# Optimization experiments

Measured on AMD Instinct MI355X. Metric: run time of the kernel, lower is better.

## Reference

```python
import jax, jax.numpy as jnp
import numpy as np

B, N, H, D2 = 2, 2048, 16, 64


def setup_inputs() -> dict:
    key = jax.random.key(0)
    k1, k2, k3 = jax.random.split(key, 3)
    keys = jax.random.normal(k1, (B, N, H, D2), dtype=jnp.float32)
    queries = jax.random.normal(k2, (B, N, H, D2), dtype=jnp.float32)
    values = jax.random.normal(k3, (B, N, H, D2), dtype=jnp.float32)
    return {"keys": keys, "queries": queries, "values": values}


def reference(keys, queries, values):
    b, n, h, d2 = keys.shape
    # Faithful to the original: torch uses .reshape (NOT transpose) to go
    # (b, n, h, d2) -> (b, h, n, d2), a pure memory reinterpretation.
    q = queries.reshape(b, h, n, d2)
    k = keys.reshape(b, h, n, d2)
    v = values.reshape(b, h, n, d2)
    scale = 1.0 / (d2 ** 0.5)
    # [b, h, n, n] attention scores
    scores = jnp.einsum('bhqd,bhkd->bhqk', q, k) * scale
    # causal mask: upper triangle (diagonal=1) set to -inf
    causal = jnp.triu(jnp.ones((n, n), dtype=bool), k=1)
    scores = jnp.where(causal, -jnp.inf, scores)
    attn = jax.nn.softmax(scores, axis=-1)
    out = jnp.einsum('bhqk,bhkd->bhqd', attn, v)
    return out.reshape(b, n, h, d2)
```

## Files before the change

kernel.cpp:

```cpp
#include <hip/hip_runtime.h>


typedef short  short4v __attribute__((ext_vector_type(4)));
typedef short  short8v __attribute__((ext_vector_type(8)));
typedef float  float4v __attribute__((ext_vector_type(4)));
typedef float  float8v __attribute__((ext_vector_type(8)));

#define NQ 2048
#define DD 64
#define KT 64
#define KP 72
#define VP 72

union U2 { unsigned int u[2]; short4v s; };
union U4 { unsigned int u[4]; short8v s; };

static __device__ __forceinline__ unsigned int pktr(float lo, float hi) {
    return __builtin_amdgcn_perm(__builtin_bit_cast(unsigned int, hi),
                                 __builtin_bit_cast(unsigned int, lo),
                                 0x07060302);
}
static __device__ __forceinline__ unsigned int pkrn(float lo, float hi) {
    unsigned int a = __builtin_bit_cast(unsigned int, hi) + 0x8000u;
    unsigned int b = __builtin_bit_cast(unsigned int, lo) + 0x8000u;
    return __builtin_amdgcn_perm(a, b, 0x07060302);
}

__global__ __launch_bounds__(512, 4) void mha_fwd_kernel(
    const float* __restrict__ Kg,
    const float* __restrict__ Qg,
    const float* __restrict__ Vg,
    float* __restrict__ Og)
{
    __shared__ __align__(16) unsigned short Klds[2][KT * KP];
    __shared__ __align__(16) unsigned short Vt[2][DD * VP];

    const int t    = threadIdx.x;
    const int lane = t & 63;
    const int wave = t >> 6;
    const int col  = lane & 15;
    const int quad = lane >> 4;

    const int b  = blockIdx.x;
    const int bh = (b & 7) * 4 + ((b >> 3) & 3);
    const int h  = b >> 5;
    const int p  = (h < 8) ? h : 23 - h;

    const int T    = (wave < 4) ? (31 - p) : p;
    const int q0   = T * 64 + (wave & 3) * 16;
    const int qg   = q0 + col;
    const int kmax = T * 64;
    const int nt   = 32 - p;

    const size_t base = (size_t)bh * NQ * DD;
    const float* Qp = Qg + base;
    const float* Kp = Kg + base;
    const float* Vp = Vg + base;
    float*       Op = Og + base;

    const float sscale = 0.125f * 1.4426950408889634f;

    const int kr = t >> 3, kc = (t & 7) * 8;
    const int vd = t & 63, vg = (t >> 6) * 8;

    short8v qf0, qf1;
    {
        float8v a = *(const float8v*)(Qp + (size_t)qg * DD + quad * 8);
        float8v c = *(const float8v*)(Qp + (size_t)qg * DD + 32 + quad * 8);
        U4 w0, w1;
#pragma unroll
        for (int i = 0; i < 4; ++i) {
            w0.u[i] = pkrn(a[2 * i] * sscale, a[2 * i + 1] * sscale);
            w1.u[i] = pkrn(c[2 * i] * sscale, c[2 * i + 1] * sscale);
        }
        qf0 = w0.s;
        qf1 = w1.s;
    }

    float l_i = 0.0f;
    float4v o[4];
#pragma unroll
    for (int d = 0; d < 4; ++d) o[d] = (float4v){0.f, 0.f, 0.f, 0.f};

    {
        float8v ka = *(const float8v*)(Kp + (size_t)kr * DD + kc);
        float vr[8];
#pragma unroll
        for (int i = 0; i < 8; ++i) vr[i] = Vp[(size_t)(vg + i) * DD + vd];
        U4 wk, wv;
#pragma unroll
        for (int i = 0; i < 4; ++i) {
            wk.u[i] = pktr(ka[2 * i], ka[2 * i + 1]);
            wv.u[i] = pktr(vr[2 * i], vr[2 * i + 1]);
        }
        *(short8v*)&Klds[0][kr * KP + kc] = wk.s;
        *(short8v*)&Vt[0][vd * VP + vg]   = wv.s;
    }
    __syncthreads();

    for (int it = 0; it < nt; ++it) {
        const int cur   = it & 1;
        const int kb    = it * KT;
        const bool stage = (it + 1 < nt);

        float8v ka;
        float vr[8];
        if (stage) {
            const int nkb = kb + KT;
            ka = *(const float8v*)(Kp + (size_t)(nkb + kr) * DD + kc);
#pragma unroll
            for (int i = 0; i < 8; ++i)
                vr[i] = Vp[(size_t)(nkb + vg + i) * DD + vd];
        }

        if (kb <= kmax) {
            __builtin_amdgcn_s_setprio(1);

            float4v sT[4];
#pragma unroll
            for (int u = 0; u < 4; ++u) {
                short8v kf0 = *(const short8v*)&Klds[cur][(u * 16 + col) * KP + quad * 8];
                short8v kf1 = *(const short8v*)&Klds[cur][(u * 16 + col) * KP + 32 + quad * 8];
                sT[u] = (float4v){0.f, 0.f, 0.f, 0.f};
                sT[u] = __builtin_amdgcn_mfma_f32_16x16x32_bf16(kf0, qf0, sT[u], 0, 0, 0);
                sT[u] = __builtin_amdgcn_mfma_f32_16x16x32_bf16(kf1, qf1, sT[u], 0, 0, 0);
            }

            if (kb == kmax) {
#pragma unroll
                for (int u = 0; u < 4; ++u)
#pragma unroll
                    for (int r = 0; r < 4; ++r) {
                        const int key = kb + u * 16 + quad * 4 + r;
                        if (key > qg) sT[u][r] = -3.0e38f;
                    }
            }

            short4v pf[4];
#pragma unroll
            for (int u = 0; u < 4; ++u) {
#pragma unroll
                for (int r = 0; r < 4; ++r) {
                    sT[u][r] = exp2f(sT[u][r]);
                    l_i += sT[u][r];
                }
                U2 w;
                w.u[0] = pktr(sT[u][0], sT[u][1]);
                w.u[1] = pktr(sT[u][2], sT[u][3]);
                pf[u] = w.s;
            }

#pragma unroll
            for (int d = 0; d < 4; ++d) {
#pragma unroll
                for (int u = 0; u < 4; ++u) {
                    short4v vf = *(const short4v*)&Vt[cur][(d * 16 + col) * VP + u * 16 + quad * 4];
                    o[d] = __builtin_amdgcn_mfma_f32_16x16x16bf16_1k(pf[u], vf, o[d], 0, 0, 0);
                }
            }

            __builtin_amdgcn_s_setprio(0);
        }

        if (stage) {
            U4 wk, wv;
#pragma unroll
            for (int i = 0; i < 4; ++i) {
                wk.u[i] = pktr(ka[2 * i], ka[2 * i + 1]);
                wv.u[i] = pktr(vr[2 * i], vr[2 * i + 1]);
            }
            *(short8v*)&Klds[cur ^ 1][kr * KP + kc] = wk.s;
            *(short8v*)&Vt[cur ^ 1][vd * VP + vg]   = wv.s;
        }

        __syncthreads();
    }

    float rs = l_i;
    rs += __shfl_xor(rs, 16);
    rs += __shfl_xor(rs, 32);
    float lv[4];
#pragma unroll
    for (int r = 0; r < 4; ++r) lv[r] = 1.0f / __shfl(rs, quad * 4 + r, 64);
#pragma unroll
    for (int r = 0; r < 4; ++r)
#pragma unroll
        for (int d = 0; d < 4; ++d)
            Op[(size_t)(q0 + quad * 4 + r) * DD + d * 16 + col] = o[d][r] * lv[r];
}

extern "C" void kernel_launch(void* const* d_in, const int* in_sizes, int n_in,
                              void* d_out, int out_size, void* d_ws, size_t ws_size,
                              hipStream_t stream) {
    const float* keys    = (const float*)d_in[0];
    const float* queries = (const float*)d_in[1];
    const float* values  = (const float*)d_in[2];
    float* out           = (float*)d_out;

    dim3 grid(2 * 16 * 16);
    dim3 block(512, 1, 1);
    mha_fwd_kernel<<<grid, block, 0, stream>>>(keys, queries, values, out);
}
```

Before: 128.8 us.

## Triple-buffer K/V tiles with two-ahead register prefetch and vectorized V reads

```diff
diff --git a/kernel.cpp b/kernel.cpp
--- a/kernel.cpp
+++ b/kernel.cpp
@@ -32,8 +32,8 @@
     const float* __restrict__ Vg,
     float* __restrict__ Og)
 {
-    __shared__ __align__(16) unsigned short Klds[2][KT * KP];
-    __shared__ __align__(16) unsigned short Vt[2][DD * VP];
+    __shared__ __align__(16) unsigned short Klds[3][KT * KP];
+    __shared__ __align__(16) unsigned short Vt[3][DD * VP];
 
     const int t    = threadIdx.x;
     const int lane = t & 63;
@@ -62,6 +62,7 @@
 
     const int kr = t >> 3, kc = (t & 7) * 8;
     const int vd = t & 63, vg = (t >> 6) * 8;
+    const int kvb = (wave & 1) * 32 + (wave >> 1) * 4;
 
     short8v qf0, qf1;
     {
@@ -82,99 +83,126 @@
 #pragma unroll
     for (int d = 0; d < 4; ++d) o[d] = (float4v){0.f, 0.f, 0.f, 0.f};
 
+    float8v kaA, kaB;
+    float   vrA[8], vrB[8];
+
     {
-        float8v ka = *(const float8v*)(Kp + (size_t)kr * DD + kc);
-        float vr[8];
-#pragma unroll
-        for (int i = 0; i < 8; ++i) vr[i] = Vp[(size_t)(vg + i) * DD + vd];
+        kaA = *(const float8v*)(Kp + (size_t)kr * DD + kc);
+#pragma unroll
+        for (int i = 0; i < 8; ++i)
+            vrA[i] = Vp[(size_t)(kvb + (i >> 2) * 16 + (i & 3)) * DD + vd];
         U4 wk, wv;
 #pragma unroll
         for (int i = 0; i < 4; ++i) {
-            wk.u[i] = pktr(ka[2 * i], ka[2 * i + 1]);
-            wv.u[i] = pktr(vr[2 * i], vr[2 * i + 1]);
+            wk.u[i] = pktr(kaA[2 * i], kaA[2 * i + 1]);
+            wv.u[i] = pktr(vrA[2 * i], vrA[2 * i + 1]);
         }
         *(short8v*)&Klds[0][kr * KP + kc] = wk.s;
         *(short8v*)&Vt[0][vd * VP + vg]   = wv.s;
+
+        kaB = *(const float8v*)(Kp + (size_t)(KT + kr) * DD + kc);
+#pragma unroll
+        for (int i = 0; i < 8; ++i)
+            vrB[i] = Vp[(size_t)(KT + kvb + (i >> 2) * 16 + (i & 3)) * DD + vd];
     }
     __syncthreads();
 
-    for (int it = 0; it < nt; ++it) {
-        const int cur   = it & 1;
-        const int kb    = it * KT;
-        const bool stage = (it + 1 < nt);
-
-        float8v ka;
-        float vr[8];
-        if (stage) {
-            const int nkb = kb + KT;
-            ka = *(const float8v*)(Kp + (size_t)(nkb + kr) * DD + kc);
-#pragma unroll
-            for (int i = 0; i < 8; ++i)
-                vr[i] = Vp[(size_t)(nkb + vg + i) * DD + vd];
+#define MHA_ITER(IT, C0, KAW, VRW, KAL, VRL)                                   \
+    {                                                                          \
+        const int kb = (IT) * KT;                                              \
+        if ((IT) + 2 < nt) {                                                   \
+            const int nkb = kb + 2 * KT;                                       \
+            KAL = *(const float8v*)(Kp + (size_t)(nkb + kr) * DD + kc);        \
+            _Pragma("unroll")                                                  \
+            for (int i = 0; i < 8; ++i)                                        \
+                VRL[i] = Vp[(size_t)(nkb + kvb + (i >> 2) * 16 + (i & 3)) * DD \
+                            + vd];                                             \
+        }                                                                      \
+        if (kb <= kmax) {                                                      \
+            __builtin_amdgcn_s_setprio(1);                                     \
+            float4v sT[4];                                                     \
+            _Pragma("unroll")                                                  \
+            for (int u = 0; u < 4; ++u) {                                      \
+                short8v kf0 = *(const short8v*)&Klds[C0][(u * 16 + col) * KP   \
+                                                         + quad * 8];          \
+                short8v kf1 = *(const short8v*)&Klds[C0][(u * 16 + col) * KP   \
+                                                         + 32 + quad * 8];     \
+                sT[u] = (float4v){0.f, 0.f, 0.f, 0.f};                         \
+                sT[u] = __builtin_amdgcn_mfma_f32_16x16x32_bf16(kf0, qf0,      \
+                                                                sT[u], 0, 0, 0);\
+                sT[u] = __builtin_amdgcn_mfma_f32_16x16x32_bf16(kf1, qf1,      \
+                                                                sT[u], 0, 0, 0);\
+            }                                                                  \
+            if (kb == kmax) {                                                  \
+                _Pragma("unroll")                                              \
+                for (int u = 0; u < 4; ++u)                                    \
+                    _Pragma("unroll")                                          \
+                    for (int r = 0; r < 4; ++r) {                              \
+                        const int key = kb + u * 16 + quad * 4 + r;            \
+                        if (key > qg) sT[u][r] = -3.0e38f;                     \
+                    }                                                          \
+            }                                                                  \
+            short4v pf[4];                                                     \
+            _Pragma("unroll")                                                  \
+            for (int u = 0; u < 4; ++u) {                                      \
+                _Pragma("unroll")                                              \
+                for (int r = 0; r < 4; ++r) {                                  \
+                    sT[u][r] = exp2f(sT[u][r]);                                \
+                    l_i += sT[u][r];                                           \
+                }                                                              \
+                U2 w;                                                          \
+                w.u[0] = pktr(sT[u][0], sT[u][1]);                             \
+                w.u[1] = pktr(sT[u][2], sT[u][3]);                             \
+                pf[u] = w.s;                                                   \
+            }                                                                  \
+            _Pragma("unroll")                                                  \
+            for (int d = 0; d < 4; ++d) {                                      \
+                short8v v01 = *(const short8v*)&Vt[C0][(d * 16 + col) * VP     \
+                                                       + quad * 16];           \
+                short8v v23 = *(const short8v*)&Vt[C0][(d * 16 + col) * VP     \
+                                                       + quad * 16 + 8];       \
+                short4v f0 = __builtin_shufflevector(v01, v01, 0, 1, 2, 3);    \
+                short4v f1 = __builtin_shufflevector(v01, v01, 4, 5, 6, 7);    \
+                short4v f2 = __builtin_shufflevector(v23, v23, 0, 1, 2, 3);    \
+                short4v f3 = __builtin_shufflevector(v23, v23, 4, 5, 6, 7);    \
+                o[d] = __builtin_amdgcn_mfma_f32_16x16x16bf16_1k(pf[0], f0,    \
+                                                                 o[d], 0, 0, 0);\
+                o[d] = __builtin_amdgcn_mfma_f32_16x16x16bf16_1k(pf[1], f1,    \
+                                                                 o[d], 0, 0, 0);\
+                o[d] = __builtin_amdgcn_mfma_f32_16x16x16bf16_1k(pf[2], f2,    \
+                                                                 o[d], 0, 0, 0);\
+                o[d] = __builtin_amdgcn_mfma_f32_16x16x16bf16_1k(pf[3], f3,    \
+                                                                 o[d], 0, 0, 0);\
+            }                                                                  \
+            __builtin_amdgcn_s_setprio(0);                                     \
+        }                                                                      \
+        if ((IT) + 1 < nt) {                                                   \
+            const int c1 = ((C0) == 2) ? 0 : (C0) + 1;                         \
+            U4 wk, wv;                                                         \
+            _Pragma("unroll")                                                  \
+            for (int i = 0; i < 4; ++i) {                                      \
+                wk.u[i] = pktr(KAW[2 * i], KAW[2 * i + 1]);                    \
+                wv.u[i] = pktr(VRW[2 * i], VRW[2 * i + 1]);                    \
+            }                                                                  \
+            *(short8v*)&Klds[c1][kr * KP + kc] = wk.s;                         \
+            *(short8v*)&Vt[c1][vd * VP + vg]   = wv.s;                         \
+        }                                                                      \
+        __syncthreads();                                                       \
+    }
+
+    {
+        int it = 0;
+        int c0 = 0;
+        while (true) {
+            MHA_ITER(it, c0, kaB, vrB, kaA, vrA);
+            ++it; c0 = (c0 == 2) ? 0 : c0 + 1;
+            if (it >= nt) break;
+            MHA_ITER(it, c0, kaA, vrA, kaB, vrB);
+            ++it; c0 = (c0 == 2) ? 0 : c0 + 1;
+            if (it >= nt) break;
         }
-
-        if (kb <= kmax) {
-            __builtin_amdgcn_s_setprio(1);
-
-            float4v sT[4];
-#pragma unroll
-            for (int u = 0; u < 4; ++u) {
-                short8v kf0 = *(const short8v*)&Klds[cur][(u * 16 + col) * KP + quad * 8];
-                short8v kf1 = *(const short8v*)&Klds[cur][(u * 16 + col) * KP + 32 + quad * 8];
-                sT[u] = (float4v){0.f, 0.f, 0.f, 0.f};
-                sT[u] = __builtin_amdgcn_mfma_f32_16x16x32_bf16(kf0, qf0, sT[u], 0, 0, 0);
-                sT[u] = __builtin_amdgcn_mfma_f32_16x16x32_bf16(kf1, qf1, sT[u], 0, 0, 0);
-            }
-
-            if (kb == kmax) {
-#pragma unroll
-                for (int u = 0; u < 4; ++u)
-#pragma unroll
-                    for (int r = 0; r < 4; ++r) {
-                        const int key = kb + u * 16 + quad * 4 + r;
-                        if (key > qg) sT[u][r] = -3.0e38f;
-                    }
-            }
-
-            short4v pf[4];
-#pragma unroll
-            for (int u = 0; u < 4; ++u) {
-#pragma unroll
-                for (int r = 0; r < 4; ++r) {
-                    sT[u][r] = exp2f(sT[u][r]);
-                    l_i += sT[u][r];
-                }
-                U2 w;
-                w.u[0] = pktr(sT[u][0], sT[u][1]);
-                w.u[1] = pktr(sT[u][2], sT[u][3]);
-                pf[u] = w.s;
-            }
-
-#pragma unroll
-            for (int d = 0; d < 4; ++d) {
-#pragma unroll
-                for (int u = 0; u < 4; ++u) {
-                    short4v vf = *(const short4v*)&Vt[cur][(d * 16 + col) * VP + u * 16 + quad * 4];
-                    o[d] = __builtin_amdgcn_mfma_f32_16x16x16bf16_1k(pf[u], vf, o[d], 0, 0, 0);
-                }
-            }
-
-            __builtin_amdgcn_s_setprio(0);
-        }
-
-        if (stage) {
-            U4 wk, wv;
-#pragma unroll
-            for (int i = 0; i < 4; ++i) {
-                wk.u[i] = pktr(ka[2 * i], ka[2 * i + 1]);
-                wv.u[i] = pktr(vr[2 * i], vr[2 * i + 1]);
-            }
-            *(short8v*)&Klds[cur ^ 1][kr * KP + kc] = wk.s;
-            *(short8v*)&Vt[cur ^ 1][vd * VP + vg]   = wv.s;
-        }
-
-        __syncthreads();
-    }
+    }
+#undef MHA_ITER
 
     float rs = l_i;
     rs += __shfl_xor(rs, 16);
```

Result: faster. 120.6 us (-6.4%).
